# Kernel optimization log

Measured on AMD Instinct MI355X. Metric: run time of the kernel, lower is better.

Reference implementation:

```python
import jax, jax.numpy as jnp
import numpy as np


def setup_inputs() -> dict:
    key = jax.random.key(0)
    k1, k2, k3, k4, k5 = jax.random.split(key, 5)
    B, T, H = 32, 4096, 256
    D = 2 * H  # encoder feature dim
    hidden = jax.random.normal(k1, (B, D), dtype=jnp.float32)
    encoder_outputs = jax.random.normal(k2, (B, T, D), dtype=jnp.float32)
    # torch nn.Linear(4H, H): weight [H, 4H], bias [H]
    W_attn = jax.random.normal(k3, (H, 4 * H), dtype=jnp.float32) * (1.0 / np.sqrt(4 * H))
    b_attn = jax.random.normal(k4, (H,), dtype=jnp.float32) * 0.01
    v = jax.random.uniform(k5, (H,), dtype=jnp.float32)  # torch.rand init
    return {"hidden": hidden, "encoder_outputs": encoder_outputs,
            "W_attn": W_attn, "b_attn": b_attn, "v": v}


def reference(hidden, encoder_outputs, W_attn, b_attn, v):
    D = hidden.shape[-1]  # 2*H
    # Split Linear(4H->H) weight into the hidden part and encoder part so we
    # never materialize the [B,T,4H] concat: cat(h,e) @ W.T == h @ Wh.T + e @ We.T
    W_h = W_attn[:, :D]   # [H, 2H]
    W_e = W_attn[:, D:]   # [H, 2H]
    h_proj = hidden @ W_h.T                     # [B, H]
    e_proj = jnp.einsum('btd,hd->bth', encoder_outputs, W_e)  # [B, T, H]
    energy = jnp.tanh(h_proj[:, None, :] + e_proj + b_attn)   # [B, T, H]
    scores = energy @ v                          # [B, T]
    attn_weights = jax.nn.softmax(scores, axis=1)  # softmax over timesteps
    context = jnp.einsum('bt,btd->bd', attn_weights, encoder_outputs)  # [B, 2H]
    return context, attn_weights
```

## Files before the change

### kernel.cpp

```cpp
#include <hip/hip_runtime.h>
#include <hip/hip_bf16.h>
#include <math.h>

#define B_  32
#define T_  4096
#define H_  256
#define D_  512

#define WS_PRE    0
#define WS_WEHI   32768
#define WS_P      294912
#define WS_ML     819200
#define WS_PCTX   827392

using short8  = __attribute__((ext_vector_type(8))) short;
using float4v = __attribute__((ext_vector_type(4))) float;

__device__ __forceinline__ unsigned cvt2_bf16(float lo, float hi) {
    union { __hip_bfloat162 h; unsigned u; } cv;
    cv.h = __float22bfloat162_rn(make_float2(lo, hi));
    return cv.u;
}
__device__ __forceinline__ short8 cvt8_bf16(const float* a) {
    union { unsigned u[4]; short8 s; } r;
    r.u[0] = cvt2_bf16(a[0], a[1]);
    r.u[1] = cvt2_bf16(a[2], a[3]);
    r.u[2] = cvt2_bf16(a[4], a[5]);
    r.u[3] = cvt2_bf16(a[6], a[7]);
    return r.s;
}

__device__ __forceinline__ float bf16_to_f32(unsigned short u) {
    unsigned v = ((unsigned)u) << 16;
    return __uint_as_float(v);
}

__device__ __forceinline__ float fast_tanh(float x) {
    float e = __expf(2.0f * x);
    return 1.0f - 2.0f * __builtin_amdgcn_rcpf(e + 1.0f);
}

__global__ __launch_bounds__(256)
void prep_kernel(const float* __restrict__ hidden,
                 const float* __restrict__ W_attn,
                 const float* __restrict__ b_attn,
                 unsigned char* __restrict__ ws) {
    int blk = blockIdx.x;
    int tid = threadIdx.x;
    if (blk < 32) {
        int b = blk, h = tid;
        const float4* hv = (const float4*)(hidden + b * D_);
        const float4* wv = (const float4*)(W_attn + (size_t)h * 1024);
        float s = 0.f;
        #pragma unroll 4
        for (int d4 = 0; d4 < D_ / 4; ++d4) {
            float4 a = hv[d4], w = wv[d4];
            s += a.x * w.x + a.y * w.y + a.z * w.z + a.w * w.w;
        }
        ((float*)(ws + WS_PRE))[b * H_ + h] = s + b_attn[h];
    } else {
        int q = (blk - 32) * 256 + tid;
        unsigned short* whi = (unsigned short*)(ws + WS_WEHI);
        #pragma unroll
        for (int i = 0; i < 4; ++i) {
            int idx4 = q + i * 8192;
            int n = idx4 >> 7, k = (idx4 & 127) << 2;
            int t = k >> 5, kin = k & 31;
            int quad = kin >> 3, e = kin & 7;
            int slot = quad ^ ((n >> 1) & 3);
            float4 w = *(const float4*)(W_attn + (size_t)n * 1024 + 512 + k);
            unsigned lo = cvt2_bf16(w.x, w.y);
            unsigned hi = cvt2_bf16(w.z, w.w);
            unsigned short* dst = whi + t * 8192 + n * 32 + slot * 8 + e;
            *(uint2*)dst = make_uint2(lo, hi);
        }
    }
}

#define BM 128
#define BN 256
#define BK 32
#define LDT 520
#define KIT 16

__global__ __launch_bounds__(512, 2)
void gemm_scores_kernel(const float* __restrict__ enc,
                        unsigned char* __restrict__ ws,
                        const float* __restrict__ v) {
    __shared__ unsigned short sE[BM * LDT];
    __shared__ float sScoreP[4][BM];
    __shared__ float sP[BM];
    __shared__ float sRed[4];

    const float*          pre = (const float*)(ws + WS_PRE);
    const unsigned short* weh = (const unsigned short*)(ws + WS_WEHI);

    int tid = threadIdx.x;
    int m0  = blockIdx.x * BM;
    int b   = m0 >> 12;

    int rowA = tid & 127, cgA = tid >> 7;
    const float* gA = enc + (size_t)(m0 + rowA) * D_ + cgA * 8;

    int wave = tid >> 6, lane = tid & 63;
    int wm = wave & 1, wn = wave >> 1;
    int quad = lane >> 4, l16 = lane & 15;

    int slotB = quad ^ ((l16 >> 1) & 3);
    const unsigned short* bBase = weh + (wn * 64 + l16) * 32 + slotB * 8;

    float4v acc[4][4] = {};

    float aX[8], aY[8];
    short8 bhA[4], bhB[4];

    {
        const float4* p0 = (const float4*)gA;
        float4 x0 = p0[0], x1 = p0[1];
        #pragma unroll
        for (int j = 0; j < 4; ++j)
            bhA[j] = *(const short8*)(bBase + j * 512);
        const float4* p1 = (const float4*)(gA + BK);
        float4 y0 = p1[0], y1 = p1[1];
        #pragma unroll
        for (int j = 0; j < 4; ++j)
            bhB[j] = *(const short8*)(bBase + 8192 + j * 512);

        float tmp[8];
        *(float4*)tmp = x0; *(float4*)(tmp + 4) = x1;
        *(short8*)&sE[rowA * LDT + cgA * 8] = cvt8_bf16(tmp);
        *(float4*)aY = y0; *(float4*)(aY + 4) = y1;
    }
    __builtin_amdgcn_s_waitcnt(0xc07f);
    __builtin_amdgcn_s_barrier();

#define K_STEP(kk, Acons, Aload, Bcur, Bnxt)                                  \
    {                                                                         \
        if ((kk) + 1 < KIT) {                                                 \
            const unsigned short* pb = bBase + ((kk) + 1) * 8192;             \
            Bnxt[0] = *(const short8*)(pb);                                   \
            Bnxt[1] = *(const short8*)(pb + 512);                             \
            Bnxt[2] = *(const short8*)(pb + 1024);                            \
            Bnxt[3] = *(const short8*)(pb + 1536);                            \
        }                                                                     \
        if ((kk) + 2 < KIT) {                                                 \
            const float4* pa = (const float4*)(gA + ((kk) + 2) * BK);         \
            *(float4*)(Aload) = pa[0]; *(float4*)((Aload) + 4) = pa[1];       \
        }                                                                     \
        short8 ah[4];                                                         \
        _Pragma("unroll")                                                     \
        for (int i = 0; i < 4; ++i) {                                         \
            int r = wm * 64 + i * 16 + l16;                                   \
            ah[i] = *(const short8*)&sE[r * LDT + (kk) * BK + quad * 8];      \
        }                                                                     \
        _Pragma("unroll")                                                     \
        for (int i = 0; i < 4; ++i)                                           \
            _Pragma("unroll")                                                 \
            for (int j = 0; j < 4; ++j)                                       \
                acc[i][j] = __builtin_amdgcn_mfma_f32_16x16x32_bf16(          \
                    ah[i], Bcur[j], acc[i][j], 0, 0, 0);                      \
        if ((kk) + 1 < KIT) {                                                 \
            *(short8*)&sE[rowA * LDT + ((kk) + 1) * BK + cgA * 8] =           \
                cvt8_bf16(Acons);                                             \
            __builtin_amdgcn_s_waitcnt(0xc07f);                               \
            __builtin_amdgcn_s_barrier();                                     \
        }                                                                     \
    }

    for (int kt = 0; kt < 8; ++kt) {
        K_STEP(2 * kt,     aY, aX, bhA, bhB)
        K_STEP(2 * kt + 1, aX, aY, bhB, bhA)
    }
#undef K_STEP

    float rowsum[4][4] = {};
    #pragma unroll
    for (int j = 0; j < 4; ++j) {
        int n = wn * 64 + j * 16 + l16;
        float pv = pre[b * H_ + n];
        float vv = v[n];
        #pragma unroll
        for (int i = 0; i < 4; ++i)
            #pragma unroll
            for (int r = 0; r < 4; ++r)
                rowsum[i][r] += fast_tanh(acc[i][j][r] + pv) * vv;
    }
    #pragma unroll
    for (int i = 0; i < 4; ++i)
        #pragma unroll
        for (int r = 0; r < 4; ++r) {
            float s = rowsum[i][r];
            s += __shfl_xor(s, 1);
            s += __shfl_xor(s, 2);
            s += __shfl_xor(s, 4);
            s += __shfl_xor(s, 8);
            rowsum[i][r] = s;
        }
    if (l16 == 0) {
        #pragma unroll
        for (int i = 0; i < 4; ++i)
            #pragma unroll
            for (int r = 0; r < 4; ++r) {
                int row = wm * 64 + i * 16 + quad * 4 + r;
                sScoreP[wn][row] = rowsum[i][r];
            }
    }
    __syncthreads();

    float sval = 0.f;
    if (tid < 128) {
        sval = sScoreP[0][tid] + sScoreP[1][tid]
             + sScoreP[2][tid] + sScoreP[3][tid];
        float m = sval;
        #pragma unroll
        for (int off = 32; off; off >>= 1) m = fmaxf(m, __shfl_xor(m, off));
        if (lane == 0) sRed[wave] = m;
    }
    __syncthreads();
    float m_blk = fmaxf(sRed[0], sRed[1]);
    if (tid < 128) {
        float p = expf(sval - m_blk);
        sP[tid] = p;
        ((float*)(ws + WS_P))[m0 + tid] = p;
        float l = p;
        #pragma unroll
        for (int off = 32; off; off >>= 1) l += __shfl_xor(l, off);
        if (lane == 0) sRed[2 + wave] = l;
    }
    __syncthreads();
    if (tid == 0) {
        float2 ml = make_float2(m_blk, sRed[2] + sRed[3]);
        ((float2*)(ws + WS_ML))[blockIdx.x] = ml;
    }

    int colg = tid & 127, rgrp = tid >> 7;
    float4 c4 = {0.f, 0.f, 0.f, 0.f};
    #pragma unroll 4
    for (int s = 0; s < 32; ++s) {
        int r = rgrp + 4 * s;
        float w = sP[r];
        uint2 raw = *(const uint2*)&sE[r * LDT + colg * 4];
        c4.x += w * bf16_to_f32((unsigned short)(raw.x & 0xffffu));
        c4.y += w * bf16_to_f32((unsigned short)(raw.x >> 16));
        c4.z += w * bf16_to_f32((unsigned short)(raw.y & 0xffffu));
        c4.w += w * bf16_to_f32((unsigned short)(raw.y >> 16));
    }
    __syncthreads();
    float4* red4 = (float4*)sE;
    red4[tid] = c4;
    __syncthreads();
    if (rgrp == 0) {
        float4 a0 = red4[colg], a1 = red4[colg + 128];
        float4 a2 = red4[colg + 256], a3 = red4[colg + 384];
        float4 o;
        o.x = a0.x + a1.x + a2.x + a3.x;
        o.y = a0.y + a1.y + a2.y + a3.y;
        o.z = a0.z + a1.z + a2.z + a3.z;
        o.w = a0.w + a1.w + a2.w + a3.w;
        ((float4*)(ws + WS_PCTX))[blockIdx.x * 128 + colg] = o;
    }
}

__global__ __launch_bounds__(512)
void finalize_kernel(const unsigned char* __restrict__ ws,
                     float* __restrict__ out_ctx,
                     float* __restrict__ out_w) {
    __shared__ float sm[32], sl[32], sscale[32];
    int b = blockIdx.x, tid = threadIdx.x;
    const float2* ml  = ((const float2*)(ws + WS_ML)) + b * 32;
    if (tid < 32) {
        float2 v = ml[tid];
        sm[tid] = v.x; sl[tid] = v.y;
    }
    __syncthreads();
    float m = -1e30f;
    #pragma unroll
    for (int i = 0; i < 32; ++i) m = fmaxf(m, sm[i]);
    float l = 0.f;
    #pragma unroll
    for (int i = 0; i < 32; ++i) l += sl[i] * expf(sm[i] - m);
    float inv = 1.0f / l;
    if (tid < 32) sscale[tid] = expf(sm[tid] - m) * inv;
    __syncthreads();

    {
        const float4* pb = (const float4*)((const float*)(ws + WS_P) + (size_t)b * T_);
        float4* wb = (float4*)(out_w + (size_t)b * T_);
        int t0 = tid * 2;
        float sc = sscale[tid >> 4];
        float4 x = pb[t0], y = pb[t0 + 1];
        x.x *= sc; x.y *= sc; x.z *= sc; x.w *= sc;
        y.x *= sc; y.y *= sc; y.z *= sc; y.w *= sc;
        wb[t0] = x; wb[t0 + 1] = y;
    }
    {
        const float* pc = (const float*)(ws + WS_PCTX) + (size_t)b * 32 * D_;
        float c = 0.f;
        #pragma unroll
        for (int i = 0; i < 32; ++i) c += pc[i * D_ + tid] * sscale[i];
        out_ctx[b * D_ + tid] = c;
    }
}

extern "C" void kernel_launch(void* const* d_in, const int* in_sizes, int n_in,
                              void* d_out, int out_size, void* d_ws, size_t ws_size,
                              hipStream_t stream) {
    const float* hidden = (const float*)d_in[0];
    const float* enc    = (const float*)d_in[1];
    const float* W_attn = (const float*)d_in[2];
    const float* b_attn = (const float*)d_in[3];
    const float* v      = (const float*)d_in[4];
    float* out = (float*)d_out;
    unsigned char* ws = (unsigned char*)d_ws;

    prep_kernel<<<64, 256, 0, stream>>>(hidden, W_attn, b_attn, ws);
    gemm_scores_kernel<<<T_ * B_ / BM, 512, 0, stream>>>(enc, ws, v);
    finalize_kernel<<<B_, 512, 0, stream>>>(ws, out, out + B_ * D_);
}
```

Before: 421.2 us.

## Halve GEMM row tile to 64 and raise occupancy to four blocks per CU

```diff
diff --git a/kernel.cpp b/kernel.cpp
--- a/kernel.cpp
+++ b/kernel.cpp
@@ -11,7 +11,7 @@
 #define WS_WEHI   32768
 #define WS_P      294912
 #define WS_ML     819200
-#define WS_PCTX   827392
+#define WS_PCTX   835584
 
 using short8  = __attribute__((ext_vector_type(8))) short;
 using float4v = __attribute__((ext_vector_type(4))) float;
@@ -21,18 +21,12 @@
     cv.h = __float22bfloat162_rn(make_float2(lo, hi));
     return cv.u;
 }
-__device__ __forceinline__ short8 cvt8_bf16(const float* a) {
-    union { unsigned u[4]; short8 s; } r;
-    r.u[0] = cvt2_bf16(a[0], a[1]);
-    r.u[1] = cvt2_bf16(a[2], a[3]);
-    r.u[2] = cvt2_bf16(a[4], a[5]);
-    r.u[3] = cvt2_bf16(a[6], a[7]);
-    return r.s;
+__device__ __forceinline__ uint2 cvt4_bf16(const float* a) {
+    return make_uint2(cvt2_bf16(a[0], a[1]), cvt2_bf16(a[2], a[3]));
 }
 
 __device__ __forceinline__ float bf16_to_f32(unsigned short u) {
-    unsigned v = ((unsigned)u) << 16;
-    return __uint_as_float(v);
+    return __uint_as_float(((unsigned)u) << 16);
 }
 
 __device__ __forceinline__ float fast_tanh(float x) {
@@ -77,20 +71,19 @@
     }
 }
 
-#define BM 128
+#define BM 64
 #define BN 256
 #define BK 32
 #define LDT 520
 #define KIT 16
 
-__global__ __launch_bounds__(512, 2)
+__global__ __launch_bounds__(512, 4)
 void gemm_scores_kernel(const float* __restrict__ enc,
                         unsigned char* __restrict__ ws,
                         const float* __restrict__ v) {
     __shared__ unsigned short sE[BM * LDT];
     __shared__ float sScoreP[4][BM];
     __shared__ float sP[BM];
-    __shared__ float sRed[4];
 
     const float*          pre = (const float*)(ws + WS_PRE);
     const unsigned short* weh = (const unsigned short*)(ws + WS_WEHI);
@@ -99,8 +92,8 @@
     int m0  = blockIdx.x * BM;
     int b   = m0 >> 12;
 
-    int rowA = tid & 127, cgA = tid >> 7;
-    const float* gA = enc + (size_t)(m0 + rowA) * D_ + cgA * 8;
+    int rowA = tid >> 3, c8 = (tid & 7) * 4;
+    const float* gA = enc + (size_t)(m0 + rowA) * D_ + c8;
 
     int wave = tid >> 6, lane = tid & 63;
     int wm = wave & 1, wn = wave >> 1;
@@ -109,27 +102,25 @@
     int slotB = quad ^ ((l16 >> 1) & 3);
     const unsigned short* bBase = weh + (wn * 64 + l16) * 32 + slotB * 8;
 
-    float4v acc[4][4] = {};
-
-    float aX[8], aY[8];
+    float4v acc[2][4] = {};
+
+    float aX[4], aY[4];
     short8 bhA[4], bhB[4];
 
     {
-        const float4* p0 = (const float4*)gA;
-        float4 x0 = p0[0], x1 = p0[1];
+        float4 x0 = *(const float4*)gA;
         #pragma unroll
         for (int j = 0; j < 4; ++j)
             bhA[j] = *(const short8*)(bBase + j * 512);
-        const float4* p1 = (const float4*)(gA + BK);
-        float4 y0 = p1[0], y1 = p1[1];
+        float4 y0 = *(const float4*)(gA + BK);
         #pragma unroll
         for (int j = 0; j < 4; ++j)
             bhB[j] = *(const short8*)(bBase + 8192 + j * 512);
 
-        float tmp[8];
-        *(float4*)tmp = x0; *(float4*)(tmp + 4) = x1;
-        *(short8*)&sE[rowA * LDT + cgA * 8] = cvt8_bf16(tmp);
-        *(float4*)aY = y0; *(float4*)(aY + 4) = y1;
+        float tmp[4];
+        *(float4*)tmp = x0;
+        *(uint2*)&sE[rowA * LDT + c8] = cvt4_bf16(tmp);
+        *(float4*)aY = y0;
     }
     __builtin_amdgcn_s_waitcnt(0xc07f);
     __builtin_amdgcn_s_barrier();
@@ -144,24 +135,23 @@
             Bnxt[3] = *(const short8*)(pb + 1536);                            \
         }                                                                     \
         if ((kk) + 2 < KIT) {                                                 \
-            const float4* pa = (const float4*)(gA + ((kk) + 2) * BK);         \
-            *(float4*)(Aload) = pa[0]; *(float4*)((Aload) + 4) = pa[1];       \
+            *(float4*)(Aload) = *(const float4*)(gA + ((kk) + 2) * BK);       \
         }                                                                     \
-        short8 ah[4];                                                         \
+        short8 ah[2];                                                         \
         _Pragma("unroll")                                                     \
-        for (int i = 0; i < 4; ++i) {                                         \
-            int r = wm * 64 + i * 16 + l16;                                   \
+        for (int i = 0; i < 2; ++i) {                                         \
+            int r = wm * 32 + i * 16 + l16;                                   \
             ah[i] = *(const short8*)&sE[r * LDT + (kk) * BK + quad * 8];      \
         }                                                                     \
         _Pragma("unroll")                                                     \
-        for (int i = 0; i < 4; ++i)                                           \
+        for (int i = 0; i < 2; ++i)                                           \
             _Pragma("unroll")                                                 \
             for (int j = 0; j < 4; ++j)                                       \
                 acc[i][j] = __builtin_amdgcn_mfma_f32_16x16x32_bf16(          \
                     ah[i], Bcur[j], acc[i][j], 0, 0, 0);                      \
         if ((kk) + 1 < KIT) {                                                 \
-            *(short8*)&sE[rowA * LDT + ((kk) + 1) * BK + cgA * 8] =           \
-                cvt8_bf16(Acons);                                             \
+            *(uint2*)&sE[rowA * LDT + ((kk) + 1) * BK + c8] =                 \
+                cvt4_bf16(Acons);                                             \
             __builtin_amdgcn_s_waitcnt(0xc07f);                               \
             __builtin_amdgcn_s_barrier();                                     \
         }                                                                     \
@@ -173,20 +163,20 @@
     }
 #undef K_STEP
 
-    float rowsum[4][4] = {};
+    float rowsum[2][4] = {};
     #pragma unroll
     for (int j = 0; j < 4; ++j) {
         int n = wn * 64 + j * 16 + l16;
         float pv = pre[b * H_ + n];
         float vv = v[n];
         #pragma unroll
-        for (int i = 0; i < 4; ++i)
+        for (int i = 0; i < 2; ++i)
             #pragma unroll
             for (int r = 0; r < 4; ++r)
                 rowsum[i][r] += fast_tanh(acc[i][j][r] + pv) * vv;
     }
     #pragma unroll
-    for (int i = 0; i < 4; ++i)
+    for (int i = 0; i < 2; ++i)
         #pragma unroll
         for (int r = 0; r < 4; ++r) {
             float s = rowsum[i][r];
@@ -198,45 +188,36 @@
         }
     if (l16 == 0) {
         #pragma unroll
-        for (int i = 0; i < 4; ++i)
+        for (int i = 0; i < 2; ++i)
             #pragma unroll
             for (int r = 0; r < 4; ++r) {
-                int row = wm * 64 + i * 16 + quad * 4 + r;
+                int row = wm * 32 + i * 16 + quad * 4 + r;
                 sScoreP[wn][row] = rowsum[i][r];
             }
     }
     __syncthreads();
 
-    float sval = 0.f;
-    if (tid < 128) {
-        sval = sScoreP[0][tid] + sScoreP[1][tid]
-             + sScoreP[2][tid] + sScoreP[3][tid];
+    if (tid < 64) {
+        float sval = sScoreP[0][tid] + sScoreP[1][tid]
+                   + sScoreP[2][tid] + sScoreP[3][tid];
         float m = sval;
         #pragma unroll
         for (int off = 32; off; off >>= 1) m = fmaxf(m, __shfl_xor(m, off));
-        if (lane == 0) sRed[wave] = m;
-    }
-    __syncthreads();
-    float m_blk = fmaxf(sRed[0], sRed[1]);
-    if (tid < 128) {
-        float p = expf(sval - m_blk);
+        float p = expf(sval - m);
         sP[tid] = p;
         ((float*)(ws + WS_P))[m0 + tid] = p;
         float l = p;
         #pragma unroll
         for (int off = 32; off; off >>= 1) l += __shfl_xor(l, off);
-        if (lane == 0) sRed[2 + wave] = l;
-    }
-    __syncthreads();
-    if (tid == 0) {
-        float2 ml = make_float2(m_blk, sRed[2] + sRed[3]);
-        ((float2*)(ws + WS_ML))[blockIdx.x] = ml;
-    }
+        if (tid == 0)
+            ((float2*)(ws + WS_ML))[blockIdx.x] = make_float2(m, l);
+    }
+    __syncthreads();
 
     int colg = tid & 127, rgrp = tid >> 7;
     float4 c4 = {0.f, 0.f, 0.f, 0.f};
     #pragma unroll 4
-    for (int s = 0; s < 32; ++s) {
+    for (int s = 0; s < 16; ++s) {
         int r = rgrp + 4 * s;
         float w = sP[r];
         uint2 raw = *(const uint2*)&sE[r * LDT + colg * 4];
@@ -265,39 +246,39 @@
 void finalize_kernel(const unsigned char* __restrict__ ws,
                      float* __restrict__ out_ctx,
                      float* __restrict__ out_w) {
-    __shared__ float sm[32], sl[32], sscale[32];
+    __shared__ float sm[64], sl[64], sscale[64];
     int b = blockIdx.x, tid = threadIdx.x;
-    const float2* ml  = ((const float2*)(ws + WS_ML)) + b * 32;
-    if (tid < 32) {
+    const float2* ml  = ((const float2*)(ws + WS_ML)) + b * 64;
+    if (tid < 64) {
         float2 v = ml[tid];
         sm[tid] = v.x; sl[tid] = v.y;
     }
     __syncthreads();
     float m = -1e30f;
     #pragma unroll
-    for (int i = 0; i < 32; ++i) m = fmaxf(m, sm[i]);
+    for (int i = 0; i < 64; ++i) m = fmaxf(m, sm[i]);
     float l = 0.f;
     #pragma unroll
-    for (int i = 0; i < 32; ++i) l += sl[i] * expf(sm[i] - m);
+    for (int i = 0; i < 64; ++i) l += sl[i] * expf(sm[i] - m);
     float inv = 1.0f / l;
-    if (tid < 32) sscale[tid] = expf(sm[tid] - m) * inv;
+    if (tid < 64) sscale[tid] = expf(sm[tid] - m) * inv;
     __syncthreads();
 
     {
         const float4* pb = (const float4*)((const float*)(ws + WS_P) + (size_t)b * T_);
         float4* wb = (float4*)(out_w + (size_t)b * T_);
         int t0 = tid * 2;
-        float sc = sscale[tid >> 4];
+        float sc = sscale[tid >> 3];
         float4 x = pb[t0], y = pb[t0 + 1];
         x.x *= sc; x.y *= sc; x.z *= sc; x.w *= sc;
         y.x *= sc; y.y *= sc; y.z *= sc; y.w *= sc;
         wb[t0] = x; wb[t0 + 1] = y;
     }
     {
-        const float* pc = (const float*)(ws + WS_PCTX) + (size_t)b * 32 * D_;
+        const float* pc = (const float*)(ws + WS_PCTX) + (size_t)b * 64 * D_;
         float c = 0.f;
         #pragma unroll
-        for (int i = 0; i < 32; ++i) c += pc[i * D_ + tid] * sscale[i];
+        for (int i = 0; i < 64; ++i) c += pc[i * D_ + tid] * sscale[i];
         out_ctx[b * D_ + tid] = c;
     }
 }
```

Measured after the change: 397.4 us, median of 2. 5.6% less time.
